# Optimization experiments

Measured on AMD Instinct MI355X. Metric: run time of the kernel, lower is better.

The kernel has to match this reference:

```python
import jax, jax.numpy as jnp
import numpy as np
import math

N = 2048       # num_nodes (dense graph)
F_IN = 256     # num_in_features
F_OUT = 256    # num_out_features
H = 8          # num_heads
LN_EPS = 1e-5

# NOTE: every e3nn FullyConnectedTensorProduct in this module maps
# (Fx0e) x irreps_sh -> (Kx0e). Only the l=0 spherical-harmonic component can
# couple scalars to scalars, and Y_0 = 1 under normalization='component'.
# Each TP is therefore exactly a linear map with a 1/sqrt(fan_in) path norm,
# and edge_direction does not enter the math at all.


def setup_inputs() -> dict:
    key = jax.random.key(0)
    ks = jax.random.split(key, 12)
    inv = 1.0 / np.sqrt(F_IN)
    return {
        "node_features": jax.random.normal(ks[0], (N, F_IN), jnp.float32),
        "edges_features_distance": jax.random.uniform(ks[1], (N, N), jnp.float32),
        "edges_features_bond": jax.random.uniform(ks[2], (N, N), jnp.float32),
        "edge_direction": jax.random.normal(ks[3], (N * N, 3), jnp.float32),
        "degree_matrix": jax.random.randint(ks[4], (N, N), 0, 2).astype(jnp.float32),
        # tensor-product weights (xavier-ish scale)
        "Wq": jax.random.normal(ks[5], (F_IN, H), jnp.float32) * inv,
        "Wk": jax.random.normal(ks[6], (F_IN, H), jnp.float32) * inv,
        "Wv": jax.random.normal(ks[7], (F_IN, F_OUT), jnp.float32) * inv,
        "w_bond": jax.random.normal(ks[8], (), jnp.float32),
        "w_bond_contrib": jax.random.normal(ks[9], (), jnp.float32),
        "w_gauss": jax.random.normal(ks[10], (), jnp.float32),
    }


def reference(node_features, edges_features_distance, edges_features_bond,
              edge_direction, degree_matrix, Wq, Wk, Wv,
              w_bond, w_bond_contrib, w_gauss):
    scale = 1.0 / jnp.sqrt(jnp.asarray(F_IN, node_features.dtype))
    # scalar-only tensor products == scaled linears (Y_0 = 1)
    q = (node_features @ Wq) * scale              # [N, H]
    k = (node_features @ Wk) * scale              # [N, H]
    v = (node_features @ Wv) * scale              # [N, F_OUT]

    # raw_attention[i,j,h] = (q_i + k_i)/sqrt(H)  (key.transpose(0,1) picks node i)
    qk = (q + k) / math.sqrt(H)                   # [N, H]
    bond = edges_features_bond * (w_bond * w_bond_contrib)   # [N, N]
    gauss = edges_features_distance * w_gauss                 # [N, N]
    raw = qk[:, None, :] + (bond + gauss)[:, :, None]          # [N, N, H]

    mask = jnp.where(degree_matrix > 0, 0.0, -1e9).astype(raw.dtype)
    scores = jax.nn.leaky_relu(raw, 0.2) + mask[:, :, None]
    # torch F.softmax without dim on a 3-D tensor -> dim=0
    attn = jax.nn.softmax(scores, axis=0)          # [N, N, H]
    # F.dropout treated as identity (eval / deterministic baseline)
    attn_mean = attn.mean(axis=2)                  # [N, N]

    # aggregated[i] = sum_j attn_mean[i,j] * v_j  (value[i,j,:] = v(node_j))
    aggregated = attn_mean @ v                     # [N, F_OUT]
    updated_nodes = jax.nn.elu(aggregated)

    # no_grad connectivity update
    un = jax.lax.stop_gradient(updated_nodes)
    sim = un @ un.T                                # [N, N]
    dd = -jax.lax.stop_gradient(edges_features_distance)
    conn = jax.nn.sigmoid(sim) * dd * jax.lax.stop_gradient(degree_matrix)
    mu = conn.mean(axis=-1, keepdims=True)
    var = conn.var(axis=-1, keepdims=True)
    conn = (conn - mu) * jax.lax.rsqrt(var + LN_EPS)
    conn = conn + conn.T
    return updated_nodes, conn
```

## Files before the change

### kernel.cpp

```cpp
#include <hip/hip_runtime.h>
#include <hip/hip_bf16.h>

#define NN 2048
#define FIN 256
#define FOUT 256
#define HH 8

typedef short bhalf8 __attribute__((ext_vector_type(8)));
typedef float f32x4  __attribute__((ext_vector_type(4)));

__device__ __forceinline__ unsigned short f2b(float f) {
    __hip_bfloat16 h = __float2bfloat16(f);
    return *reinterpret_cast<unsigned short*>(&h);
}
__device__ __forceinline__ float b2f(unsigned short u) {
    __hip_bfloat16 h = *reinterpret_cast<__hip_bfloat16*>(&u);
    return __bfloat162float(h);
}

__global__ __launch_bounds__(256) void k1_qkv(
    const float* __restrict__ x, const float* __restrict__ Wq,
    const float* __restrict__ Wk, const float* __restrict__ Wv,
    float* __restrict__ v, float* __restrict__ qk)
{
    const int ib = blockIdx.x * 4;
    const int t  = threadIdx.x;
    __shared__ float xs[4][FIN];
    __shared__ float part[256];
    #pragma unroll
    for (int n = 0; n < 4; ++n) xs[n][t] = x[(long)(ib+n)*FIN + t];
    __syncthreads();
    float a0 = 0.f, a1 = 0.f, a2 = 0.f, a3 = 0.f;
    #pragma unroll 4
    for (int c = 0; c < FIN; ++c) {
        const float wv = Wv[c*FOUT + t];
        a0 = fmaf(xs[0][c], wv, a0); a1 = fmaf(xs[1][c], wv, a1);
        a2 = fmaf(xs[2][c], wv, a2); a3 = fmaf(xs[3][c], wv, a3);
    }
    v[(ib+0)*FOUT + t] = a0 * 0.0625f;
    v[(ib+1)*FOUT + t] = a1 * 0.0625f;
    v[(ib+2)*FOUT + t] = a2 * 0.0625f;
    v[(ib+3)*FOUT + t] = a3 * 0.0625f;
    {
        const int n = t >> 6, h = t & 7, seg = (t >> 3) & 7;
        float a = 0.f;
        for (int c = seg*32; c < seg*32 + 32; ++c)
            a = fmaf(xs[n][c], Wq[c*HH + h] + Wk[c*HH + h], a);
        part[t] = a;
    }
    __syncthreads();
    if (t < 32) {
        const int n = t >> 3, h = t & 7;
        float a = 0.f;
        #pragma unroll
        for (int s2 = 0; s2 < 8; ++s2) a += part[n*64 + s2*8 + h];
        qk[(ib+n)*HH + h] = a * (0.0625f * 0.35355339059327373f);
    }
}

__global__ __launch_bounds__(256) void k1b_vT(
    const float* __restrict__ v, unsigned short* __restrict__ vtb)
{
    const int k0 = blockIdx.x * 64;
    const int f0 = blockIdx.y * 64;
    const int t  = threadIdx.x;
    __shared__ float LT[64][68];
    const int r  = t >> 4;
    const int c4 = (t & 15) * 4;
    #pragma unroll
    for (int p = 0; p < 4; ++p) {
        const float4 q = *(const float4*)&v[(k0 + r + p*16)*FOUT + f0 + c4];
        LT[c4+0][r + p*16] = q.x; LT[c4+1][r + p*16] = q.y;
        LT[c4+2][r + p*16] = q.z; LT[c4+3][r + p*16] = q.w;
    }
    __syncthreads();
    #pragma unroll
    for (int p = 0; p < 4; ++p) {
        const int fr = r + p*16;
        ushort4 ub;
        ub.x = f2b(LT[fr][c4+0]); ub.y = f2b(LT[fr][c4+1]);
        ub.z = f2b(LT[fr][c4+2]); ub.w = f2b(LT[fr][c4+3]);
        *(ushort4*)&vtb[(long)(f0 + fr)*NN + k0 + c4] = ub;
    }
}

__global__ __launch_bounds__(256) void k2_denom(
    const float* __restrict__ bond, const float* __restrict__ dist,
    const float* __restrict__ deg, const float* __restrict__ qk,
    const float* __restrict__ wb, const float* __restrict__ wbc,
    const float* __restrict__ wg, float* __restrict__ D,
    unsigned short* __restrict__ fbuf, unsigned short* __restrict__ ddb)
{
    const float cb = wb[0] * wbc[0];
    const float cg = wg[0];
    const int t  = threadIdx.x;
    const int tx = t & 63;
    const int ty = t >> 6;
    const int j0 = blockIdx.x * 256;
    const int i0 = blockIdx.y * 64;
    const int j  = j0 + tx*4;
    __shared__ float qs[64*8];
    __shared__ float red[4][2048];
    for (int p = t; p < 512; p += 256) qs[p] = qk[i0*8 + p];
    __syncthreads();
    float acc[4][8];
    #pragma unroll
    for (int jj = 0; jj < 4; ++jj)
        #pragma unroll
        for (int h = 0; h < 8; ++h) acc[jj][h] = 0.f;
    const int ibase = i0 + ty*16;
    for (int ii = 0; ii < 16; ++ii) {
        const long idx = (long)(ibase + ii)*NN + j;
        const float4 dv = *(const float4*)&dist[idx];
        const float4 bv = *(const float4*)&bond[idx];
        const float4 gv = *(const float4*)&deg[idx];
        ushort4 fb, db;
        fb.x = f2b((gv.x > 0.f) ? fmaf(cb, bv.x, cg*dv.x) : -__builtin_inff());
        fb.y = f2b((gv.y > 0.f) ? fmaf(cb, bv.y, cg*dv.y) : -__builtin_inff());
        fb.z = f2b((gv.z > 0.f) ? fmaf(cb, bv.z, cg*dv.z) : -__builtin_inff());
        fb.w = f2b((gv.w > 0.f) ? fmaf(cb, bv.w, cg*dv.w) : -__builtin_inff());
        db.x = f2b(-dv.x * gv.x); db.y = f2b(-dv.y * gv.y);
        db.z = f2b(-dv.z * gv.z); db.w = f2b(-dv.w * gv.w);
        *(ushort4*)&fbuf[idx] = fb;
        *(ushort4*)&ddb[idx]  = db;
        float s[4];
        s[0] = b2f(fb.x); s[1] = b2f(fb.y); s[2] = b2f(fb.z); s[3] = b2f(fb.w);
        const float* qrow = &qs[(ty*16 + ii)*8];
        #pragma unroll
        for (int h = 0; h < 8; ++h) {
            const float q = qrow[h];
            #pragma unroll
            for (int jj = 0; jj < 4; ++jj) {
                float r = q + s[jj];
                r = fmaxf(r, 0.2f*r);
                acc[jj][h] += __expf(r);
            }
        }
    }
    #pragma unroll
    for (int jj = 0; jj < 4; ++jj)
        #pragma unroll
        for (int h = 0; h < 8; ++h) red[ty][(tx*4 + jj)*8 + h] = acc[jj][h];
    __syncthreads();
    for (int p = t; p < 2048; p += 256) {
        const float ssum = red[0][p] + red[1][p] + red[2][p] + red[3][p];
        atomicAdd(&D[j0*8 + p], ssum);
    }
}

__global__ __launch_bounds__(256) void k3_attnmean(
    const unsigned short* __restrict__ fbuf, const float* __restrict__ qk,
    const float* __restrict__ D, unsigned short* __restrict__ amb)
{
    const int t  = threadIdx.x;
    const int tx = t & 63;
    const int ty = t >> 6;
    const int j0 = blockIdx.x * 256;
    const int i0 = blockIdx.y * 64;
    const int j  = j0 + tx*4;
    __shared__ float qs[64*8];
    for (int p = t; p < 512; p += 256) qs[p] = qk[i0*8 + p];
    __syncthreads();
    float invD[4][8];
    #pragma unroll
    for (int jj = 0; jj < 4; ++jj) {
        const float4 d0 = *(const float4*)&D[(j + jj)*8 + 0];
        const float4 d1 = *(const float4*)&D[(j + jj)*8 + 4];
        invD[jj][0] = 0.125f / fmaxf(d0.x, 1e-30f);
        invD[jj][1] = 0.125f / fmaxf(d0.y, 1e-30f);
        invD[jj][2] = 0.125f / fmaxf(d0.z, 1e-30f);
        invD[jj][3] = 0.125f / fmaxf(d0.w, 1e-30f);
        invD[jj][4] = 0.125f / fmaxf(d1.x, 1e-30f);
        invD[jj][5] = 0.125f / fmaxf(d1.y, 1e-30f);
        invD[jj][6] = 0.125f / fmaxf(d1.z, 1e-30f);
        invD[jj][7] = 0.125f / fmaxf(d1.w, 1e-30f);
    }
    const int ibase = i0 + ty*16;
    for (int ii = 0; ii < 16; ++ii) {
        const long idx = (long)(ibase + ii)*NN + j;
        const ushort4 fb = *(const ushort4*)&fbuf[idx];
        float s[4];
        s[0] = b2f(fb.x); s[1] = b2f(fb.y); s[2] = b2f(fb.z); s[3] = b2f(fb.w);
        float o[4] = {0.f, 0.f, 0.f, 0.f};
        const float* qrow = &qs[(ty*16 + ii)*8];
        #pragma unroll
        for (int h = 0; h < 8; ++h) {
            const float q = qrow[h];
            #pragma unroll
            for (int jj = 0; jj < 4; ++jj) {
                float r = q + s[jj];
                r = fmaxf(r, 0.2f*r);
                o[jj] = fmaf(__expf(r), invD[jj][h], o[jj]);
            }
        }
        ushort4 ob;
        ob.x = f2b(o[0]); ob.y = f2b(o[1]); ob.z = f2b(o[2]); ob.w = f2b(o[3]);
        *(ushort4*)&amb[idx] = ob;
    }
}

__global__ __launch_bounds__(128) void k4_aggr(
    const unsigned short* __restrict__ amb,
    const unsigned short* __restrict__ vtb,
    float* __restrict__ out0, unsigned short* __restrict__ unb)
{
    const int i0 = blockIdx.x * 32;
    const int f0 = blockIdx.y * 32;
    const int w  = threadIdx.x >> 6;
    const int l  = threadIdx.x & 63;
    const int lm = l & 15, lq = l >> 4;
    const int iw = i0 + w*16;
    f32x4 acc0 = {0,0,0,0}, acc1 = {0,0,0,0};
    const unsigned short* arow  = &amb[(long)(iw + lm)*NN + lq*8];
    const unsigned short* brow0 = &vtb[(long)(f0 + lm)*NN + lq*8];
    const unsigned short* brow1 = &vtb[(long)(f0 + 16 + lm)*NN + lq*8];
    #pragma unroll 4
    for (int kk = 0; kk < NN; kk += 32) {
        const bhalf8 a  = *(const bhalf8*)&arow[kk];
        const bhalf8 b0 = *(const bhalf8*)&brow0[kk];
        const bhalf8 b1 = *(const bhalf8*)&brow1[kk];
        acc0 = __builtin_amdgcn_mfma_f32_16x16x32_bf16(a, b0, acc0, 0, 0, 0);
        acc1 = __builtin_amdgcn_mfma_f32_16x16x32_bf16(a, b1, acc1, 0, 0, 0);
    }
    #pragma unroll
    for (int r = 0; r < 4; ++r) {
        const int i = iw + lq*4 + r;
        float s0 = acc0[r], s1 = acc1[r];
        s0 = (s0 > 0.f) ? s0 : (__expf(s0) - 1.f);
        s1 = (s1 > 0.f) ? s1 : (__expf(s1) - 1.f);
        out0[(long)i*FOUT + f0 + lm]      = s0;
        out0[(long)i*FOUT + f0 + 16 + lm] = s1;
        unb[(long)i*FOUT + f0 + lm]       = f2b(s0);
        unb[(long)i*FOUT + f0 + 16 + lm]  = f2b(s1);
    }
}

__global__ __launch_bounds__(256) void k5_sim(
    const unsigned short* __restrict__ unb, const unsigned short* __restrict__ ddb,
    unsigned short* __restrict__ c0,
    float* __restrict__ rowsum, float* __restrict__ rowsq)
{
    const int i0 = blockIdx.y * 64;
    const int j0 = blockIdx.x * 64;
    const int w  = threadIdx.x >> 6;
    const int l  = threadIdx.x & 63;
    const int lm = l & 15, lq = l >> 4;
    const int iw = i0 + w*16;
    f32x4 acc[4] = {f32x4{0,0,0,0}, f32x4{0,0,0,0}, f32x4{0,0,0,0}, f32x4{0,0,0,0}};
    for (int kk = 0; kk < FOUT; kk += 32) {
        const bhalf8 a = *(const bhalf8*)&unb[(long)(iw + lm)*FOUT + kk + lq*8];
        #pragma unroll
        for (int c = 0; c < 4; ++c) {
            const bhalf8 b = *(const bhalf8*)&unb[(long)(j0 + c*16 + lm)*FOUT + kk + lq*8];
            acc[c] = __builtin_amdgcn_mfma_f32_16x16x32_bf16(a, b, acc[c], 0, 0, 0);
        }
    }
    float srow[4] = {0.f,0.f,0.f,0.f}, qrow[4] = {0.f,0.f,0.f,0.f};
    #pragma unroll
    for (int c = 0; c < 4; ++c) {
        #pragma unroll
        for (int r = 0; r < 4; ++r) {
            const int i = iw + lq*4 + r;
            const int j = j0 + c*16 + lm;
            const long idx = (long)i*NN + j;
            const float sg = 1.f / (1.f + __expf(-acc[c][r]));
            const float val = sg * b2f(ddb[idx]);
            c0[idx] = f2b(val);
            srow[r] += val;
            qrow[r] = fmaf(val, val, qrow[r]);
        }
    }
    #pragma unroll
    for (int r = 0; r < 4; ++r) {
        #pragma unroll
        for (int m = 8; m >= 1; m >>= 1) {
            srow[r] += __shfl_xor(srow[r], m, 64);
            qrow[r] += __shfl_xor(qrow[r], m, 64);
        }
        if (lm == 0) {
            atomicAdd(&rowsum[iw + lq*4 + r], srow[r]);
            atomicAdd(&rowsq[iw + lq*4 + r],  qrow[r]);
        }
    }
}

__global__ void k6_stats(const float* __restrict__ rowsum,
                         const float* __restrict__ rowsq,
                         float* __restrict__ mu, float* __restrict__ rs)
{
    const int i = blockIdx.x*256 + threadIdx.x;
    if (i < NN) {
        const float m = rowsum[i] * (1.f/NN);
        const float var = rowsq[i] * (1.f/NN) - m*m;
        mu[i] = m;
        rs[i] = rsqrtf(var + 1e-5f);
    }
}

__global__ __launch_bounds__(256) void k7_conn(
    const unsigned short* __restrict__ c0, const float* __restrict__ mu,
    const float* __restrict__ rs, float* __restrict__ out1)
{
    const int i0 = blockIdx.y * 64;
    const int j0 = blockIdx.x * 64;
    const int t  = threadIdx.x;
    __shared__ float LT[64][68];
    __shared__ float muj[64], rsj[64];
    const int r  = t >> 4;
    const int c4 = (t & 15) * 4;
    if (t < 64)        muj[t] = mu[j0 + t];
    else if (t < 128)  rsj[t-64] = rs[j0 + t - 64];
    #pragma unroll
    for (int p = 0; p < 4; ++p) {
        const int jl = r + p*16;
        const ushort4 q = *(const ushort4*)&c0[(long)(j0 + jl)*NN + i0 + c4];
        LT[c4+0][jl] = b2f(q.x); LT[c4+1][jl] = b2f(q.y);
        LT[c4+2][jl] = b2f(q.z); LT[c4+3][jl] = b2f(q.w);
    }
    __syncthreads();
    #pragma unroll
    for (int p = 0; p < 4; ++p) {
        const int rr = r + p*16;
        const int i  = i0 + rr;
        const ushort4 xb = *(const ushort4*)&c0[(long)i*NN + j0 + c4];
        const float mi = mu[i], ri = rs[i];
        float4 o;
        o.x = (b2f(xb.x) - mi)*ri + (LT[rr][c4+0] - muj[c4+0])*rsj[c4+0];
        o.y = (b2f(xb.y) - mi)*ri + (LT[rr][c4+1] - muj[c4+1])*rsj[c4+1];
        o.z = (b2f(xb.z) - mi)*ri + (LT[rr][c4+2] - muj[c4+2])*rsj[c4+2];
        o.w = (b2f(xb.w) - mi)*ri + (LT[rr][c4+3] - muj[c4+3])*rsj[c4+3];
        *(float4*)&out1[(long)i*NN + j0 + c4] = o;
    }
}

extern "C" void kernel_launch(void* const* d_in, const int* in_sizes, int n_in,
                              void* d_out, int out_size, void* d_ws, size_t ws_size,
                              hipStream_t stream)
{
    const float* x    = (const float*)d_in[0];
    const float* dist = (const float*)d_in[1];
    const float* bond = (const float*)d_in[2];
    const float* deg  = (const float*)d_in[4];
    const float* Wq   = (const float*)d_in[5];
    const float* Wk   = (const float*)d_in[6];
    const float* Wv   = (const float*)d_in[7];
    const float* wb   = (const float*)d_in[8];
    const float* wbc  = (const float*)d_in[9];
    const float* wg   = (const float*)d_in[10];

    float* out0 = (float*)d_out;
    float* out1 = out0 + (size_t)NN*FOUT;

    char* w = (char*)d_ws;
    unsigned short* fbuf = (unsigned short*)(w);
    unsigned short* c0   = (unsigned short*)(w);
    unsigned short* amb  = (unsigned short*)(w +  8388608);
    unsigned short* ddb  = (unsigned short*)(w + 16777216);
    float* v       = (float*)(w + 33554432);
    unsigned short* vtb = (unsigned short*)(w + 35651584);
    unsigned short* unb = (unsigned short*)(w + 36700160);
    float* qk      = (float*)(w + 37748736);
    float* D       = (float*)(w + 37814272);
    float* rowsum  = (float*)(w + 37879808);
    float* rowsq   = (float*)(w + 37888000);
    float* mu      = (float*)(w + 37896192);
    float* rs      = (float*)(w + 37904384);

    hipMemsetAsync(D, 0, 65536 + 8192 + 8192, stream);

    k1_qkv<<<NN/4, 256, 0, stream>>>(x, Wq, Wk, Wv, v, qk);
    dim3 g1b(NN/64, FOUT/64);
    k1b_vT<<<g1b, 256, 0, stream>>>(v, vtb);
    dim3 g23(NN/256, NN/64);
    k2_denom<<<g23, 256, 0, stream>>>(bond, dist, deg, qk, wb, wbc, wg, D, fbuf, ddb);
    k3_attnmean<<<g23, 256, 0, stream>>>(fbuf, qk, D, amb);
    dim3 g4(NN/32, FOUT/32);
    k4_aggr<<<g4, 128, 0, stream>>>(amb, vtb, out0, unb);
    dim3 g5(NN/64, NN/64);
    k5_sim<<<g5, 256, 0, stream>>>(unb, ddb, c0, rowsum, rowsq);
    k6_stats<<<8, 256, 0, stream>>>(rowsum, rowsq, mu, rs);
    k7_conn<<<g5, 256, 0, stream>>>(c0, mu, rs, out1);
}
```

Measured before the change: 250.8 us.

## Fuse memset, transpose and stats kernels; retile denom, attn and aggregation grids

The memset is folded into k1, which also writes v directly as transposed bf16, so the separate transpose kernel goes away. The k6 stats kernel is merged into k7, which now computes mu and rsqrt itself. k2 and k3 move to 32-row tiles, doubling the grid, and k4 moves to one 16x16 MFMA tile per wave with 256-thread blocks. The aim is fewer launches and better occupancy, at the cost of uncoalesced stride-NN stores of vtb in k1 and more D atomics from the larger k2 grid.

Result: faster. 240.5 us (-4.1%).

```diff
diff --git a/kernel.cpp b/kernel.cpp
--- a/kernel.cpp
+++ b/kernel.cpp
@@ -21,10 +21,17 @@
 __global__ __launch_bounds__(256) void k1_qkv(
     const float* __restrict__ x, const float* __restrict__ Wq,
     const float* __restrict__ Wk, const float* __restrict__ Wv,
-    float* __restrict__ v, float* __restrict__ qk)
+    unsigned short* __restrict__ vtb, float* __restrict__ qk,
+    float* __restrict__ D, float* __restrict__ rowsum, float* __restrict__ rowsq)
 {
     const int ib = blockIdx.x * 4;
     const int t  = threadIdx.x;
+    {
+        const int tp = blockIdx.x*256 + t;
+        if      (tp < 16384) D[tp] = 0.f;
+        else if (tp < 18432) rowsum[tp - 16384] = 0.f;
+        else if (tp < 20480) rowsq [tp - 18432] = 0.f;
+    }
     __shared__ float xs[4][FIN];
     __shared__ float part[256];
     #pragma unroll
@@ -37,10 +44,10 @@
         a0 = fmaf(xs[0][c], wv, a0); a1 = fmaf(xs[1][c], wv, a1);
         a2 = fmaf(xs[2][c], wv, a2); a3 = fmaf(xs[3][c], wv, a3);
     }
-    v[(ib+0)*FOUT + t] = a0 * 0.0625f;
-    v[(ib+1)*FOUT + t] = a1 * 0.0625f;
-    v[(ib+2)*FOUT + t] = a2 * 0.0625f;
-    v[(ib+3)*FOUT + t] = a3 * 0.0625f;
+    ushort4 uv;
+    uv.x = f2b(a0 * 0.0625f); uv.y = f2b(a1 * 0.0625f);
+    uv.z = f2b(a2 * 0.0625f); uv.w = f2b(a3 * 0.0625f);
+    *(ushort4*)&vtb[(long)t*NN + ib] = uv;
     {
         const int n = t >> 6, h = t & 7, seg = (t >> 3) & 7;
         float a = 0.f;
@@ -58,32 +65,6 @@
     }
 }
 
-__global__ __launch_bounds__(256) void k1b_vT(
-    const float* __restrict__ v, unsigned short* __restrict__ vtb)
-{
-    const int k0 = blockIdx.x * 64;
-    const int f0 = blockIdx.y * 64;
-    const int t  = threadIdx.x;
-    __shared__ float LT[64][68];
-    const int r  = t >> 4;
-    const int c4 = (t & 15) * 4;
-    #pragma unroll
-    for (int p = 0; p < 4; ++p) {
-        const float4 q = *(const float4*)&v[(k0 + r + p*16)*FOUT + f0 + c4];
-        LT[c4+0][r + p*16] = q.x; LT[c4+1][r + p*16] = q.y;
-        LT[c4+2][r + p*16] = q.z; LT[c4+3][r + p*16] = q.w;
-    }
-    __syncthreads();
-    #pragma unroll
-    for (int p = 0; p < 4; ++p) {
-        const int fr = r + p*16;
-        ushort4 ub;
-        ub.x = f2b(LT[fr][c4+0]); ub.y = f2b(LT[fr][c4+1]);
-        ub.z = f2b(LT[fr][c4+2]); ub.w = f2b(LT[fr][c4+3]);
-        *(ushort4*)&vtb[(long)(f0 + fr)*NN + k0 + c4] = ub;
-    }
-}
-
 __global__ __launch_bounds__(256) void k2_denom(
     const float* __restrict__ bond, const float* __restrict__ dist,
     const float* __restrict__ deg, const float* __restrict__ qk,
@@ -97,19 +78,21 @@
     const int tx = t & 63;
     const int ty = t >> 6;
     const int j0 = blockIdx.x * 256;
-    const int i0 = blockIdx.y * 64;
+    const int i0 = blockIdx.y * 32;
     const int j  = j0 + tx*4;
-    __shared__ float qs[64*8];
+    __shared__ float qs[32*8];
     __shared__ float red[4][2048];
-    for (int p = t; p < 512; p += 256) qs[p] = qk[i0*8 + p];
+    if (t < 256) {  }
+    for (int p = t; p < 256; p += 256) qs[p] = qk[i0*8 + p];
     __syncthreads();
     float acc[4][8];
     #pragma unroll
     for (int jj = 0; jj < 4; ++jj)
         #pragma unroll
         for (int h = 0; h < 8; ++h) acc[jj][h] = 0.f;
-    const int ibase = i0 + ty*16;
-    for (int ii = 0; ii < 16; ++ii) {
+    const int ibase = i0 + ty*8;
+    #pragma unroll
+    for (int ii = 0; ii < 8; ++ii) {
         const long idx = (long)(ibase + ii)*NN + j;
         const float4 dv = *(const float4*)&dist[idx];
         const float4 bv = *(const float4*)&bond[idx];
@@ -125,7 +108,7 @@
         *(ushort4*)&ddb[idx]  = db;
         float s[4];
         s[0] = b2f(fb.x); s[1] = b2f(fb.y); s[2] = b2f(fb.z); s[3] = b2f(fb.w);
-        const float* qrow = &qs[(ty*16 + ii)*8];
+        const float* qrow = &qs[(ty*8 + ii)*8];
         #pragma unroll
         for (int h = 0; h < 8; ++h) {
             const float q = qrow[h];
@@ -156,33 +139,26 @@
     const int tx = t & 63;
     const int ty = t >> 6;
     const int j0 = blockIdx.x * 256;
-    const int i0 = blockIdx.y * 64;
+    const int i0 = blockIdx.y * 32;
     const int j  = j0 + tx*4;
-    __shared__ float qs[64*8];
-    for (int p = t; p < 512; p += 256) qs[p] = qk[i0*8 + p];
+    __shared__ float qs[32*8];
+    for (int p = t; p < 256; p += 256) qs[p] = qk[i0*8 + p];
     __syncthreads();
     float invD[4][8];
     #pragma unroll
-    for (int jj = 0; jj < 4; ++jj) {
-        const float4 d0 = *(const float4*)&D[(j + jj)*8 + 0];
-        const float4 d1 = *(const float4*)&D[(j + jj)*8 + 4];
-        invD[jj][0] = 0.125f / fmaxf(d0.x, 1e-30f);
-        invD[jj][1] = 0.125f / fmaxf(d0.y, 1e-30f);
-        invD[jj][2] = 0.125f / fmaxf(d0.z, 1e-30f);
-        invD[jj][3] = 0.125f / fmaxf(d0.w, 1e-30f);
-        invD[jj][4] = 0.125f / fmaxf(d1.x, 1e-30f);
-        invD[jj][5] = 0.125f / fmaxf(d1.y, 1e-30f);
-        invD[jj][6] = 0.125f / fmaxf(d1.z, 1e-30f);
-        invD[jj][7] = 0.125f / fmaxf(d1.w, 1e-30f);
-    }
-    const int ibase = i0 + ty*16;
-    for (int ii = 0; ii < 16; ++ii) {
+    for (int jj = 0; jj < 4; ++jj)
+        #pragma unroll
+        for (int h = 0; h < 8; ++h)
+            invD[jj][h] = 0.125f / fmaxf(D[(j + jj)*8 + h], 1e-30f);
+    const int ibase = i0 + ty*8;
+    #pragma unroll
+    for (int ii = 0; ii < 8; ++ii) {
         const long idx = (long)(ibase + ii)*NN + j;
         const ushort4 fb = *(const ushort4*)&fbuf[idx];
         float s[4];
         s[0] = b2f(fb.x); s[1] = b2f(fb.y); s[2] = b2f(fb.z); s[3] = b2f(fb.w);
         float o[4] = {0.f, 0.f, 0.f, 0.f};
-        const float* qrow = &qs[(ty*16 + ii)*8];
+        const float* qrow = &qs[(ty*8 + ii)*8];
         #pragma unroll
         for (int h = 0; h < 8; ++h) {
             const float q = qrow[h];
@@ -199,39 +175,33 @@
     }
 }
 
-__global__ __launch_bounds__(128) void k4_aggr(
+__global__ __launch_bounds__(256) void k4_aggr(
     const unsigned short* __restrict__ amb,
     const unsigned short* __restrict__ vtb,
     float* __restrict__ out0, unsigned short* __restrict__ unb)
 {
-    const int i0 = blockIdx.x * 32;
-    const int f0 = blockIdx.y * 32;
-    const int w  = threadIdx.x >> 6;
-    const int l  = threadIdx.x & 63;
-    const int lm = l & 15, lq = l >> 4;
-    const int iw = i0 + w*16;
-    f32x4 acc0 = {0,0,0,0}, acc1 = {0,0,0,0};
-    const unsigned short* arow  = &amb[(long)(iw + lm)*NN + lq*8];
-    const unsigned short* brow0 = &vtb[(long)(f0 + lm)*NN + lq*8];
-    const unsigned short* brow1 = &vtb[(long)(f0 + 16 + lm)*NN + lq*8];
+    const int w = threadIdx.x >> 6, lane = threadIdx.x & 63;
+    const int vw = blockIdx.x*4 + w;
+    const int it = vw >> 4;
+    const int f0 = (vw & 15) * 16;
+    const int lm = lane & 15, lq = lane >> 4;
+    const unsigned short* arow = &amb[(long)(it*16 + lm)*NN + lq*8];
+    const unsigned short* brow = &vtb[(long)(f0 + lm)*NN + lq*8];
+    f32x4 acc = {0.f, 0.f, 0.f, 0.f};
     #pragma unroll 4
     for (int kk = 0; kk < NN; kk += 32) {
-        const bhalf8 a  = *(const bhalf8*)&arow[kk];
-        const bhalf8 b0 = *(const bhalf8*)&brow0[kk];
-        const bhalf8 b1 = *(const bhalf8*)&brow1[kk];
-        acc0 = __builtin_amdgcn_mfma_f32_16x16x32_bf16(a, b0, acc0, 0, 0, 0);
-        acc1 = __builtin_amdgcn_mfma_f32_16x16x32_bf16(a, b1, acc1, 0, 0, 0);
+        const bhalf8 a = *(const bhalf8*)&arow[kk];
+        const bhalf8 b = *(const bhalf8*)&brow[kk];
+        acc = __builtin_amdgcn_mfma_f32_16x16x32_bf16(a, b, acc, 0, 0, 0);
     }
     #pragma unroll
     for (int r = 0; r < 4; ++r) {
-        const int i = iw + lq*4 + r;
-        float s0 = acc0[r], s1 = acc1[r];
-        s0 = (s0 > 0.f) ? s0 : (__expf(s0) - 1.f);
-        s1 = (s1 > 0.f) ? s1 : (__expf(s1) - 1.f);
-        out0[(long)i*FOUT + f0 + lm]      = s0;
-        out0[(long)i*FOUT + f0 + 16 + lm] = s1;
-        unb[(long)i*FOUT + f0 + lm]       = f2b(s0);
-        unb[(long)i*FOUT + f0 + 16 + lm]  = f2b(s1);
+        const int i = it*16 + lq*4 + r;
+        const int f = f0 + lm;
+        float s = acc[r];
+        s = (s > 0.f) ? s : (__expf(s) - 1.f);
+        out0[(long)i*FOUT + f] = s;
+        unb [(long)i*FOUT + f] = f2b(s);
     }
 }
 
@@ -279,37 +249,32 @@
         }
         if (lm == 0) {
             atomicAdd(&rowsum[iw + lq*4 + r], srow[r]);
-            atomicAdd(&rowsq[iw + lq*4 + r],  qrow[r]);
-        }
-    }
-}
-
-__global__ void k6_stats(const float* __restrict__ rowsum,
-                         const float* __restrict__ rowsq,
-                         float* __restrict__ mu, float* __restrict__ rs)
-{
-    const int i = blockIdx.x*256 + threadIdx.x;
-    if (i < NN) {
-        const float m = rowsum[i] * (1.f/NN);
-        const float var = rowsq[i] * (1.f/NN) - m*m;
-        mu[i] = m;
-        rs[i] = rsqrtf(var + 1e-5f);
+            atomicAdd(&rowsq [iw + lq*4 + r], qrow[r]);
+        }
     }
 }
 
 __global__ __launch_bounds__(256) void k7_conn(
-    const unsigned short* __restrict__ c0, const float* __restrict__ mu,
-    const float* __restrict__ rs, float* __restrict__ out1)
+    const unsigned short* __restrict__ c0, const float* __restrict__ rowsum,
+    const float* __restrict__ rowsq, float* __restrict__ out1)
 {
     const int i0 = blockIdx.y * 64;
     const int j0 = blockIdx.x * 64;
     const int t  = threadIdx.x;
     __shared__ float LT[64][68];
-    __shared__ float muj[64], rsj[64];
+    __shared__ float mui[64], rii[64], muj[64], rsj[64];
     const int r  = t >> 4;
     const int c4 = (t & 15) * 4;
-    if (t < 64)        muj[t] = mu[j0 + t];
-    else if (t < 128)  rsj[t-64] = rs[j0 + t - 64];
+    if (t < 64) {
+        const float m = rowsum[j0 + t] * (1.f/NN);
+        muj[t] = m;
+        rsj[t] = rsqrtf(rowsq[j0 + t]*(1.f/NN) - m*m + 1e-5f);
+    } else if (t < 128) {
+        const int rr = t - 64;
+        const float m = rowsum[i0 + rr] * (1.f/NN);
+        mui[rr] = m;
+        rii[rr] = rsqrtf(rowsq[i0 + rr]*(1.f/NN) - m*m + 1e-5f);
+    }
     #pragma unroll
     for (int p = 0; p < 4; ++p) {
         const int jl = r + p*16;
@@ -323,7 +288,7 @@
         const int rr = r + p*16;
         const int i  = i0 + rr;
         const ushort4 xb = *(const ushort4*)&c0[(long)i*NN + j0 + c4];
-        const float mi = mu[i], ri = rs[i];
+        const float mi = mui[rr], ri = rii[rr];
         float4 o;
         o.x = (b2f(xb.x) - mi)*ri + (LT[rr][c4+0] - muj[c4+0])*rsj[c4+0];
         o.y = (b2f(xb.y) - mi)*ri + (LT[rr][c4+1] - muj[c4+1])*rsj[c4+1];
@@ -352,32 +317,22 @@
     float* out1 = out0 + (size_t)NN*FOUT;
 
     char* w = (char*)d_ws;
-    unsigned short* fbuf = (unsigned short*)(w);
-    unsigned short* c0   = (unsigned short*)(w);
+    unsigned short* fbuf_c0 = (unsigned short*)(w);
     unsigned short* amb  = (unsigned short*)(w +  8388608);
     unsigned short* ddb  = (unsigned short*)(w + 16777216);
-    float* v       = (float*)(w + 33554432);
-    unsigned short* vtb = (unsigned short*)(w + 35651584);
-    unsigned short* unb = (unsigned short*)(w + 36700160);
-    float* qk      = (float*)(w + 37748736);
-    float* D       = (float*)(w + 37814272);
-    float* rowsum  = (float*)(w + 37879808);
-    float* rowsq   = (float*)(w + 37888000);
-    float* mu      = (float*)(w + 37896192);
-    float* rs      = (float*)(w + 37904384);
-
-    hipMemsetAsync(D, 0, 65536 + 8192 + 8192, stream);
-
-    k1_qkv<<<NN/4, 256, 0, stream>>>(x, Wq, Wk, Wv, v, qk);
-    dim3 g1b(NN/64, FOUT/64);
-    k1b_vT<<<g1b, 256, 0, stream>>>(v, vtb);
-    dim3 g23(NN/256, NN/64);
-    k2_denom<<<g23, 256, 0, stream>>>(bond, dist, deg, qk, wb, wbc, wg, D, fbuf, ddb);
-    k3_attnmean<<<g23, 256, 0, stream>>>(fbuf, qk, D, amb);
-    dim3 g4(NN/32, FOUT/32);
-    k4_aggr<<<g4, 128, 0, stream>>>(amb, vtb, out0, unb);
+    unsigned short* vtb  = (unsigned short*)(w + 25165824);
+    unsigned short* unb  = (unsigned short*)(w + 26214400);
+    float* qk      = (float*)(w + 27262976);
+    float* D       = (float*)(w + 27328512);
+    float* rowsum  = (float*)(w + 27394048);
+    float* rowsq   = (float*)(w + 27402240);
+
+    k1_qkv<<<NN/4, 256, 0, stream>>>(x, Wq, Wk, Wv, vtb, qk, D, rowsum, rowsq);
+    dim3 g23(NN/256, NN/32);
+    k2_denom<<<g23, 256, 0, stream>>>(bond, dist, deg, qk, wb, wbc, wg, D, fbuf_c0, ddb);
+    k3_attnmean<<<g23, 256, 0, stream>>>(fbuf_c0, qk, D, amb);
+    k4_aggr<<<NN/4, 256, 0, stream>>>(amb, vtb, out0, unb);
     dim3 g5(NN/64, NN/64);
-    k5_sim<<<g5, 256, 0, stream>>>(unb, ddb, c0, rowsum, rowsq);
-    k6_stats<<<8, 256, 0, stream>>>(rowsum, rowsq, mu, rs);
-    k7_conn<<<g5, 256, 0, stream>>>(c0, mu, rs, out1);
-}
+    k5_sim<<<g5, 256, 0, stream>>>(unb, ddb, fbuf_c0, rowsum, rowsq);
+    k7_conn<<<g5, 256, 0, stream>>>(fbuf_c0, rowsum, rowsq, out1);
+}
```
